# Optimization experiments

Hardware: AMD Instinct MI355X
Metric: run time of the kernel (lower is better)

Reference implementation:

```python
import jax, jax.numpy as jnp
import numpy as np

B, S, D, H, KV, HD = 2, 1024, 4096, 32, 8, 128
GROUP = H // KV


def setup_inputs() -> dict:
    key = jax.random.key(0)
    ks = jax.random.split(key, 9)
    x = jax.random.normal(ks[0], (B, S, D), dtype=jnp.float32)
    # RoPE tables: [max_seq_len, head_dim] (half-duplicated frequencies)
    pos = jnp.arange(S, dtype=jnp.float32)
    inv_freq = 1.0 / (10000.0 ** (jnp.arange(0, HD, 2, dtype=jnp.float32) / HD))
    freqs = pos[:, None] * inv_freq[None, :]            # [S, HD/2]
    emb = jnp.concatenate([freqs, freqs], axis=-1)      # [S, HD]
    cos, sin = jnp.cos(emb), jnp.sin(emb)
    # causal mask: True = masked
    mask = jnp.triu(jnp.ones((S, S), dtype=bool), 1)[None, None]  # [1,1,S,S]
    def qw(k, o, i):
        return jax.random.randint(k, (o, i), -127, 128, dtype=jnp.int8)
    wq = qw(ks[1], H * HD, D)
    wk = qw(ks[2], KV * HD, D)
    wv = qw(ks[3], KV * HD, D)
    wo = qw(ks[4], D, H * HD)
    sq = jnp.float32(0.02); sk = jnp.float32(0.02)
    sv = jnp.float32(0.02); so = jnp.float32(0.02)
    bq = jax.random.normal(ks[5], (H * HD,), jnp.float32) * 0.01
    bk = jax.random.normal(ks[6], (KV * HD,), jnp.float32) * 0.01
    bv = jax.random.normal(ks[7], (KV * HD,), jnp.float32) * 0.01
    return dict(x=x, mask=mask, cos=cos, sin=sin,
                wq=wq, bq=bq, sq=sq, wk=wk, bk=bk, sk=sk,
                wv=wv, bv=bv, sv=sv, wo=wo, so=so, start_pos=0)


def _deq_linear(x, w_int8, scale, bias):
    # dequantize-on-the-fly int8 linear: y = x @ (w.astype * scale).T + b
    w = w_int8.astype(x.dtype) * scale                  # [O, I]
    y = jnp.einsum('bsi,oi->bso', x, w)
    return y if bias is None else y + bias


def _rope(x, cos, sin, offset):
    # x: [b, s, h, hd]
    hd = x.shape[-1]
    x1, x2 = x[..., : hd // 2], x[..., hd // 2 :]
    s_len = x.shape[1]
    c = cos[offset : offset + s_len][None, :, None, :]
    s = sin[offset : offset + s_len][None, :, None, :]
    rotated = jnp.concatenate([-x2, x1], axis=-1)
    return (x * c + rotated * s).astype(x.dtype)


def reference(x, mask, cos, sin, wq, bq, sq, wk, bk, sk, wv, bv, sv, wo, so, start_pos):
    b, seq, _ = x.shape
    xq = _deq_linear(x, wq, sq, bq).reshape(b, seq, H, HD)
    xk = _deq_linear(x, wk, sk, bk).reshape(b, seq, KV, HD)
    xv = _deq_linear(x, wv, sv, bv).reshape(b, seq, KV, HD)
    xq = _rope(xq, cos, sin, start_pos)
    xk = _rope(xk, cos, sin, start_pos)
    # KV cache: start_pos=0 prefill -> cache[:start_pos+seq] == (xk, xv)
    kv_idx = jnp.arange(H) // GROUP                      # q head -> kv head
    keys = xk[:, :, kv_idx, :]                           # [b, kv_len, H, hd]
    values = xv[:, :, kv_idx, :]
    scores = jnp.einsum('bqhd,bkhd->bhqk', xq, keys) / np.sqrt(HD).astype(np.float32)
    scores = jnp.where(mask, -jnp.inf, scores)
    probs = jax.nn.softmax(scores, axis=-1)
    out = jnp.einsum('bhqk,bkhd->bqhd', probs, values).reshape(b, seq, H * HD)
    return _deq_linear(out, wo, so, None)
```

## Files before the change

kernel.cpp:

```cpp
#include <hip/hip_runtime.h>
#include <hip/hip_bf16.h>
#include <hip/hip_fp16.h>
#include <cstdint>

typedef _Float16 f16;
typedef _Float16 f16x8 __attribute__((ext_vector_type(8)));
typedef _Float16 f16x4 __attribute__((ext_vector_type(4)));
typedef float f32x4 __attribute__((ext_vector_type(4)));

#define DEV_INLINE __device__ __forceinline__

DEV_INLINE void async_ld16(const void* g, void* l) {
  __builtin_amdgcn_global_load_lds((const __attribute__((address_space(1))) void*)g,
                                   (__attribute__((address_space(3))) void*)l, 16, 0, 0);
}

template <int N>
DEV_INLINE void wait_vm() {
  static_assert(N >= 0 && N <= 12, "gate range");
  if constexpr (N == 0)  asm volatile("s_waitcnt vmcnt(0)" ::: "memory");
  if constexpr (N == 1)  asm volatile("s_waitcnt vmcnt(1)" ::: "memory");
  if constexpr (N == 2)  asm volatile("s_waitcnt vmcnt(2)" ::: "memory");
  if constexpr (N == 3)  asm volatile("s_waitcnt vmcnt(3)" ::: "memory");
  if constexpr (N == 4)  asm volatile("s_waitcnt vmcnt(4)" ::: "memory");
  if constexpr (N == 5)  asm volatile("s_waitcnt vmcnt(5)" ::: "memory");
  if constexpr (N == 6)  asm volatile("s_waitcnt vmcnt(6)" ::: "memory");
  if constexpr (N == 7)  asm volatile("s_waitcnt vmcnt(7)" ::: "memory");
  if constexpr (N == 8)  asm volatile("s_waitcnt vmcnt(8)" ::: "memory");
  if constexpr (N == 9)  asm volatile("s_waitcnt vmcnt(9)" ::: "memory");
  if constexpr (N == 10) asm volatile("s_waitcnt vmcnt(10)" ::: "memory");
  if constexpr (N == 11) asm volatile("s_waitcnt vmcnt(11)" ::: "memory");
  if constexpr (N == 12) asm volatile("s_waitcnt vmcnt(12)" ::: "memory");
}
DEV_INLINE void lgk0() {
  asm volatile("s_waitcnt lgkmcnt(0)" ::: "memory");
  __builtin_amdgcn_sched_barrier(0);
}

__global__ __launch_bounds__(256) void k_prep_all(
    const float* __restrict__ x,
    const int* __restrict__ wq, const int* __restrict__ wk, const int* __restrict__ wv,
    const float* __restrict__ bq, const float* __restrict__ bk, const float* __restrict__ bv,
    const float* __restrict__ sq, const float* __restrict__ sk, const float* __restrict__ sv,
    f16* __restrict__ acat, f16* __restrict__ wcat,
    float* __restrict__ bias_cat, float* __restrict__ scale_cat) {
  const int bid = blockIdx.x;
  if (bid < 8192) {
    int i = (bid * 256 + threadIdx.x) * 4;
    float4 v = *(const float4*)&x[i];
    int row = i >> 12, col = i & 4095;
    f16 h0 = (f16)v.x, h1 = (f16)v.y, h2 = (f16)v.z, h3 = (f16)v.w;
    f16x4 hi = {h0, h1, h2, h3};
    f16x4 lo = {(f16)(v.x - (float)h0), (f16)(v.y - (float)h1),
                (f16)(v.z - (float)h2), (f16)(v.w - (float)h3)};
    size_t base = (size_t)row * 8192 + col;
    *(f16x4*)&acat[base] = hi;
    *(f16x4*)&acat[base + 4096] = lo;
  } else {
    int i = (bid - 8192) * 256 + threadIdx.x;
    if (i < 6291456) {
      int e = i * 4, row = e >> 12, col = e & 4095;
      int4 v;
      if (row < 4096)      v = *(const int4*)&wq[(size_t)row * 4096 + col];
      else if (row < 5120) v = *(const int4*)&wk[(size_t)(row - 4096) * 4096 + col];
      else                 v = *(const int4*)&wv[(size_t)(row - 5120) * 4096 + col];
      f16x4 o = {(f16)(float)v.x, (f16)(float)v.y, (f16)(float)v.z, (f16)(float)v.w};
      *(f16x4*)&wcat[e] = o;
    }
    if (i < 6144) {
      float b, s;
      if (i < 4096)      { b = bq[i];        s = sq[0]; }
      else if (i < 5120) { b = bk[i - 4096]; s = sk[0]; }
      else               { b = bv[i - 5120]; s = sv[0]; }
      bias_cat[i] = b;
      scale_cat[i] = s;
    }
  }
}

__global__ __launch_bounds__(256) void k_cast_i32_f16(const int* __restrict__ w,
                                                      f16* __restrict__ out, int n) {
  int i = (blockIdx.x * 256 + threadIdx.x) * 4;
  if (i >= n) return;
  int4 v = *(const int4*)&w[i];
  f16x4 o = {(f16)(float)v.x, (f16)(float)v.y, (f16)(float)v.z, (f16)(float)v.w};
  *(f16x4*)&out[i] = o;
}

template <int BM, int BN, int MODE>
__global__ __launch_bounds__(512) void k_gemm9(
    const f16* __restrict__ A, const f16* __restrict__ W,
    f16* __restrict__ o_hi, f16* __restrict__ o_lo, float* __restrict__ o_f32,
    const float* __restrict__ scale_vec, const float* __restrict__ bias_vec,
    const float* __restrict__ scale_scalar,
    const float* __restrict__ cosT, const float* __restrict__ sinT,
    const int* __restrict__ sp,
    int N, int K, int kmask, int ldw, int nym) {
  constexpr int WM = 2, WN = 4;
  constexpr int MR = BM / WM / 16;
  constexpr int NR = BN / WN / 16;
  constexpr int AKC = BM * 64;
  constexpr int BKC = BN * 64;
  constexpr int SLOT = 2 * (AKC + BKC);
  constexpr int LAH = AKC / 8192;
  constexpr int LBH = BKC / 8192;
  constexpr int GS = 2 * (LAH + LBH);
  constexpr int G1 = LAH + LBH;
  extern __shared__ __align__(16) char lds[];

  const int t = threadIdx.x, w = t >> 6, ln = t & 63;
  const int lr = ln & 15, lg = ln >> 4;
  const int wn = w & 3, wm = w >> 2;

  const int nwg = gridDim.x;
  const int q8 = nwg >> 3, r8 = nwg & 7;
  const int xcd = blockIdx.x & 7, bidx = blockIdx.x >> 3;
  const int sid = (xcd < r8 ? xcd * (q8 + 1) : r8 * (q8 + 1) + (xcd - r8) * q8) + bidx;
  const int m0 = (sid % nym) * BM;
  const int n0 = (sid / nym) * BN;

  const f16* aSrc[LAH];
  const f16* bSrc[LBH];
#pragma unroll
  for (int l = 0; l < LAH; l++) {
    int ci = l * 512 + t, row = ci >> 2, c = ci & 3;
    aSrc[l] = A + (size_t)(m0 + row) * K + (c ^ ((row >> 1) & 3)) * 8;
  }
#pragma unroll
  for (int l = 0; l < LBH; l++) {
    int ci = l * 512 + t, row = ci >> 2, c = ci & 3;
    bSrc[l] = W + (size_t)(n0 + row) * ldw + (c ^ ((row >> 1) & 3)) * 8;
  }

  f32x4 acc[MR][NR] = {};
  f16x8 af[MR], bfa[NR];

  auto stageA = [&](int tt, int kc) {
    char* dst = lds + (tt & 1) * SLOT + kc * AKC;
    const int ko = tt * 64 + kc * 32;
#pragma unroll
    for (int l = 0; l < LAH; l++)
      async_ld16(aSrc[l] + ko, dst + (l * 512 + w * 64) * 16);
  };
  auto stageB = [&](int tt, int kc) {
    char* dst = lds + (tt & 1) * SLOT + 2 * AKC + kc * BKC;
    const int ko = ((tt * 64) & kmask) + kc * 32;
#pragma unroll
    for (int l = 0; l < LBH; l++)
      async_ld16(bSrc[l] + ko, dst + (l * 512 + w * 64) * 16);
  };
  auto readA = [&](int tt, int kc) {
    const char* base = lds + (tt & 1) * SLOT + kc * AKC;
#pragma unroll
    for (int mf = 0; mf < MR; mf++) {
      const int row = wm * (BM / WM) + mf * 16 + lr;
      af[mf] = *(const f16x8*)(base + row * 64 + (lg ^ ((row >> 1) & 3)) * 16);
    }
  };
  auto readBall = [&](int tt, int kc) {
    const char* base = lds + (tt & 1) * SLOT + 2 * AKC + kc * BKC;
#pragma unroll
    for (int nf = 0; nf < NR; nf++) {
      const int row = wn * (BN / WN) + nf * 16 + lr;
      bfa[nf] = *(const f16x8*)(base + row * 64 + (lg ^ ((row >> 1) & 3)) * 16);
    }
  };
  auto mma = [&]() {
    __builtin_amdgcn_s_setprio(1);
#pragma unroll
    for (int m = 0; m < MR; m++)
#pragma unroll
      for (int n = 0; n < NR; n++)
        acc[m][n] = __builtin_amdgcn_mfma_f32_16x16x32_f16(af[m], bfa[n], acc[m][n], 0, 0, 0);
    __builtin_amdgcn_s_setprio(0);
  };
  auto bar = [&]() { __builtin_amdgcn_s_barrier(); };

  const int NT = K >> 6;
  stageA(0, 0); stageB(0, 0); stageA(0, 1); stageB(0, 1);
  stageA(1, 0); stageB(1, 0);
  wait_vm<GS>();
  bar();

  for (int tt = 0; tt + 2 < NT; ++tt) {
    stageA(tt + 1, 1); stageB(tt + 1, 1);
    readA(tt, 0); readBall(tt, 0);
    wait_vm<GS>();
    bar(); lgk0(); mma(); bar();
    stageA(tt + 2, 0); stageB(tt + 2, 0);
    readA(tt, 1); readBall(tt, 1);
    wait_vm<GS>();
    bar(); lgk0(); mma(); bar();
  }
  {
    const int tt = NT - 2;
    stageA(tt + 1, 1); stageB(tt + 1, 1);
    readA(tt, 0); readBall(tt, 0);
    wait_vm<GS>();
    bar(); lgk0(); mma(); bar();
    readA(tt, 1); readBall(tt, 1);
    wait_vm<G1>();
    bar(); lgk0(); mma(); bar();
  }
  {
    const int tt = NT - 1;
    readA(tt, 0); readBall(tt, 0);
    wait_vm<0>();
    bar(); lgk0(); mma(); bar();
    readA(tt, 1); readBall(tt, 1);
    lgk0(); mma();
  }

  if constexpr (MODE == 0) {
    float* xch = (float*)lds;
    const int sp0 = sp[0];
    for (int pass = 0; pass < 2; ++pass) {
      bar();
      if (wm == pass) {
#pragma unroll
        for (int n = 0; n < NR; n++) {
          const int col = wn * (BN / WN) + n * 16 + lr;
          const float sc = scale_vec[n0 + col];
          const float bs = bias_vec[n0 + col];
#pragma unroll
          for (int m = 0; m < MR; m++)
#pragma unroll
            for (int r2 = 0; r2 < 4; r2++) {
              const int row = m * 16 + lg * 4 + r2;
              xch[row * 385 + col] = acc[m][n][r2] * sc + bs;
            }
        }
      }
      bar();
      for (int j = 0; j < (64 * BN) / 512; j++) {
        const int idx = j * 512 + t;
        const int r = idx / BN;
        const int c = idx - r * BN;
        const int gr = m0 + pass * 64 + r;
        const int gcol = n0 + c;
        float v = xch[r * 385 + c];
        float o;
        if (gcol < 5120) {
          const int q = c & 127;
          const int pos = (gr & 1023) + sp0;
          const float cs = cosT[pos * 128 + q];
          const float sn = sinT[pos * 128 + q];
          const float vp = xch[r * 385 + ((q < 64) ? c + 64 : c - 64)];
          o = (q < 64) ? v * cs - vp * sn : v * cs + vp * sn;
        } else {
          o = v;
        }
        f16 h = (f16)o;
        o_hi[(size_t)gr * N + gcol] = h;
        o_lo[(size_t)gr * N + gcol] = (f16)(o - (float)h);
      }
    }
  } else {
#pragma unroll
    for (int n = 0; n < NR; n++) {
      const int col = n0 + wn * (BN / WN) + n * 16 + lr;
      const float sc = scale_scalar[0];
#pragma unroll
      for (int m = 0; m < MR; m++)
#pragma unroll
        for (int r2 = 0; r2 < 4; r2++) {
          const int row = m0 + wm * (BM / WM) + m * 16 + lg * 4 + r2;
          o_f32[(size_t)row * N + col] = acc[m][n][r2] * sc;
        }
    }
  }
}

__global__ __launch_bounds__(512) void k_attn6(const f16* __restrict__ XH,
                                               const f16* __restrict__ XL,
                                               f16* __restrict__ out) {
  __shared__ __align__(16) f16 KsH[32 * 152];
  __shared__ __align__(16) f16 KsL[32 * 152];
  __shared__ __align__(16) f16 VT[128 * 40];
  __shared__ __align__(16) f16 Pb[8 * 16 * 40];
  const int t = threadIdx.x, w = t >> 6, l = t & 63;
  const int lr = l & 15, lg = l >> 4;
  const int id = blockIdx.x;
  const int kvh = id & 7;
  const int j = id >> 3;
  const int half = j >> 5;
  const int jj = j & 31;
  const int qb = half ? 7 - (jj >> 3) : (jj >> 3);
  const int hg = jj & 3;
  const int b = (jj >> 2) & 1;
  const int h = kvh * 4 + hg;
  const int q0 = qb * 128;
  const size_t rs_ = 6144;
  const f16* Qh = XH + ((size_t)(b * 1024 + q0)) * rs_ + h * 128;
  const f16* Ql_ = XL + ((size_t)(b * 1024 + q0)) * rs_ + h * 128;
  const f16* KhG = XH + ((size_t)(b * 1024)) * rs_ + 4096 + kvh * 128;
  const f16* KlG = XL + ((size_t)(b * 1024)) * rs_ + 4096 + kvh * 128;
  const f16* VG = XH + ((size_t)(b * 1024)) * rs_ + 5120 + kvh * 128;

  f16x8 qh[4], ql[4];
  {
    size_t qoff = (size_t)(w * 16 + lr) * rs_ + lg * 8;
#pragma unroll
    for (int c = 0; c < 4; c++) {
      qh[c] = *(const f16x8*)(Qh + qoff + c * 32);
      ql[c] = *(const f16x8*)(Ql_ + qoff + c * 32);
    }
  }
  f32x4 accd[8] = {};
  float m_r[4], l_r[4];
#pragma unroll
  for (int r = 0; r < 4; r++) { m_r[r] = -1e30f; l_r[r] = 0.f; }

  const int krow_s = t >> 4, kch = t & 15;
  const int vrow_s = t & 31, vd8 = t >> 5;
  f16x8 khr, klr, vr;
  auto loadKV = [&](int kv0) {
    size_t go = (size_t)(kv0 + krow_s) * rs_ + kch * 8;
    khr = *(const f16x8*)(KhG + go);
    klr = *(const f16x8*)(KlG + go);
    vr = *(const f16x8*)(VG + (size_t)(kv0 + vrow_s) * rs_ + vd8 * 8);
  };
  auto writeKV = [&]() {
    *(f16x8*)&KsH[krow_s * 152 + kch * 8] = khr;
    *(f16x8*)&KsL[krow_s * 152 + kch * 8] = klr;
#pragma unroll
    for (int jj2 = 0; jj2 < 8; jj2++) VT[(vd8 * 8 + jj2) * 40 + vrow_s] = vr[jj2];
  };

  const int nkv = q0 + 128;
  const int NT = nkv >> 5;
  loadKV(0);
  wait_vm<0>();
  writeKV();
  __syncthreads();

  for (int tt = 0; tt < NT; ++tt) {
    const int kv0 = tt * 32;
    const bool pf = (tt + 1 < NT);
    if (pf) {
      loadKV(kv0 + 32);
      __builtin_amdgcn_sched_barrier(0);
    }

    f32x4 sc[2] = {};
#pragma unroll
    for (int cb = 0; cb < 2; cb++)
#pragma unroll
      for (int c = 0; c < 4; c++) {
        const f16x8 kh = *(const f16x8*)&KsH[(cb * 16 + lr) * 152 + c * 32 + lg * 8];
        const f16x8 kl = *(const f16x8*)&KsL[(cb * 16 + lr) * 152 + c * 32 + lg * 8];
        sc[cb] = __builtin_amdgcn_mfma_f32_16x16x32_f16(qh[c], kh, sc[cb], 0, 0, 0);
        sc[cb] = __builtin_amdgcn_mfma_f32_16x16x32_f16(qh[c], kl, sc[cb], 0, 0, 0);
        sc[cb] = __builtin_amdgcn_mfma_f32_16x16x32_f16(ql[c], kh, sc[cb], 0, 0, 0);
      }

    const float scale = 0.088388347648318447f;
    float alpha[4], pv[2][4];
#pragma unroll
    for (int r = 0; r < 4; r++) {
      const int qg = q0 + w * 16 + lg * 4 + r;
      float mx = -1e30f;
#pragma unroll
      for (int cb = 0; cb < 2; cb++) {
        const int kg = kv0 + cb * 16 + lr;
        float s = sc[cb][r] * scale;
        s = (kg <= qg) ? s : -1e30f;
        pv[cb][r] = s;
        mx = fmaxf(mx, s);
      }
      mx = fmaxf(mx, __shfl_xor(mx, 1));
      mx = fmaxf(mx, __shfl_xor(mx, 2));
      mx = fmaxf(mx, __shfl_xor(mx, 4));
      mx = fmaxf(mx, __shfl_xor(mx, 8));
      const float mn = fmaxf(m_r[r], mx);
      alpha[r] = __expf(m_r[r] - mn);
      m_r[r] = mn;
      float rsum = 0.f;
#pragma unroll
      for (int cb = 0; cb < 2; cb++) {
        const int kg = kv0 + cb * 16 + lr;
        const float p = (kg <= qg) ? __expf(pv[cb][r] - mn) : 0.f;
        pv[cb][r] = p;
        rsum += p;
      }
      rsum += __shfl_xor(rsum, 1);
      rsum += __shfl_xor(rsum, 2);
      rsum += __shfl_xor(rsum, 4);
      rsum += __shfl_xor(rsum, 8);
      l_r[r] = l_r[r] * alpha[r] + rsum;
    }

    f16* Pw = &Pb[w * 16 * 40];
#pragma unroll
    for (int r = 0; r < 4; r++)
#pragma unroll
      for (int cb = 0; cb < 2; cb++)
        Pw[(lg * 4 + r) * 40 + cb * 16 + lr] = (f16)pv[cb][r];
    const f16x8 pf_ = *(const f16x8*)&Pw[lr * 40 + lg * 8];

#pragma unroll
    for (int dc = 0; dc < 8; dc++) {
      const f16x8 vf = *(const f16x8*)&VT[(dc * 16 + lr) * 40 + lg * 8];
#pragma unroll
      for (int r = 0; r < 4; r++) accd[dc][r] *= alpha[r];
      accd[dc] = __builtin_amdgcn_mfma_f32_16x16x32_f16(pf_, vf, accd[dc], 0, 0, 0);
    }

    __syncthreads();
    if (pf) writeKV();
    __syncthreads();
  }

#pragma unroll
  for (int dc = 0; dc < 8; dc++)
#pragma unroll
    for (int r = 0; r < 4; r++) {
      const int row = b * 1024 + q0 + w * 16 + lg * 4 + r;
      out[(size_t)row * 4096 + h * 128 + dc * 16 + lr] = (f16)(accd[dc][r] / l_r[r]);
    }
}

extern "C" void kernel_launch(void* const* d_in, const int* in_sizes, int n_in,
                              void* d_out, int out_size, void* d_ws, size_t ws_size,
                              hipStream_t stream) {
  const float* x = (const float*)d_in[0];
  const float* cosT = (const float*)d_in[2];
  const float* sinT = (const float*)d_in[3];
  const int* wq = (const int*)d_in[4];
  const float* bq = (const float*)d_in[5];
  const float* sq = (const float*)d_in[6];
  const int* wk = (const int*)d_in[7];
  const float* bk = (const float*)d_in[8];
  const float* sk = (const float*)d_in[9];
  const int* wv = (const int*)d_in[10];
  const float* bv = (const float*)d_in[11];
  const float* sv = (const float*)d_in[12];
  const int* wo = (const int*)d_in[13];
  const float* so = (const float*)d_in[14];
  const int* sp = (const int*)d_in[15];

  char* ws = (char*)d_ws;
  f16* Acat = (f16*)ws;
  f16* Wcat = (f16*)(ws + 33554432);
  f16* XH = (f16*)(ws + 83886080);
  f16* XL = (f16*)(ws + 109051904);
  f16* AO = (f16*)(ws + 134217728);
  float* biasv = (float*)(ws + 150994944);
  float* scalev = (float*)(ws + 151019520);

  hipFuncSetAttribute(reinterpret_cast<const void*>(&k_gemm9<128, 384, 0>),
                      hipFuncAttributeMaxDynamicSharedMemorySize, 131072);
  hipFuncSetAttribute(reinterpret_cast<const void*>(&k_gemm9<128, 256, 1>),
                      hipFuncAttributeMaxDynamicSharedMemorySize, 98304);

  k_prep_all<<<32768, 256, 0, stream>>>(x, wq, wk, wv, bq, bk, bv, sq, sk, sv,
                                        Acat, Wcat, biasv, scalev);

  k_gemm9<128, 384, 0><<<256, 512, 131072, stream>>>(
      Acat, Wcat, XH, XL, nullptr, scalev, biasv, nullptr, cosT, sinT, sp,
      6144, 8192, 4095, 4096, 16);

  f16* Wo_ = Acat;
  k_cast_i32_f16<<<16384, 256, 0, stream>>>(wo, Wo_, 16777216);

  k_attn6<<<512, 512, 0, stream>>>(XH, XL, AO);

  k_gemm9<128, 256, 1><<<256, 512, 98304, stream>>>(
      AO, Wo_, nullptr, nullptr, (float*)d_out, nullptr, nullptr, so,
      nullptr, nullptr, nullptr, 4096, 4096, 0x7fffffff, 4096, 16);
}
```

Before: 421.4 us.

## Replace QKV GEMM with dedicated 64x384-tile kernel and simpler double-buffered pipeline

Adds a dedicated QKV projection kernel that uses 64x384 tiles, 256 threads and 512 workgroups instead of 128x384 tiles with 512 threads. It uses a two-slot LDS pipeline with a K-step of 32 and an XCD-aware block-to-tile mapping, and keeps the fused bias, scale, RoPE and hi/lo f16 split epilogue. The generic GEMM is reduced to the output-projection mode only. The smaller tile and smaller LDS footprint are meant to improve occupancy and load balance across CUs, at the cost of less data reuse per tile and more redundant weight loads.

```diff
diff --git a/kernel.cpp b/kernel.cpp
--- a/kernel.cpp
+++ b/kernel.cpp
@@ -87,14 +87,154 @@
   *(f16x4*)&out[i] = o;
 }
 
+__global__ __launch_bounds__(256) void k_qkv10(
+    const f16* __restrict__ A, const f16* __restrict__ W,
+    f16* __restrict__ o_hi, f16* __restrict__ o_lo,
+    const float* __restrict__ scale_vec, const float* __restrict__ bias_vec,
+    const float* __restrict__ cosT, const float* __restrict__ sinT,
+    const int* __restrict__ sp) {
+  constexpr int BM = 64, BN = 384, N = 6144, K = 8192, kmask = 4095, ldw = 4096;
+  constexpr int MR = 4, NR = 6;
+  constexpr int AKC = BM * 64;
+  constexpr int BKC = BN * 64;
+  constexpr int SLOT = AKC + BKC;
+  constexpr int LB = 6;
+  extern __shared__ __align__(16) char lds[];
+
+  const int t = threadIdx.x, w = t >> 6, ln = t & 63;
+  const int lr = ln & 15, lg = ln >> 4;
+  const int wn = w;
+
+  const int xcd = blockIdx.x & 7, bidx = blockIdx.x >> 3;
+  const int sid = xcd * 64 + bidx;
+  const int m0 = (sid & 31) * BM;
+  const int n0 = (sid >> 5) * BN;
+
+  const f16* aSrc;
+  const f16* bSrc[LB];
+  {
+    int row = t >> 2, c = t & 3;
+    aSrc = A + (size_t)(m0 + row) * K + (c ^ ((row >> 1) & 3)) * 8;
+  }
+#pragma unroll
+  for (int l = 0; l < LB; l++) {
+    int ci = l * 256 + t, row = ci >> 2, c = ci & 3;
+    bSrc[l] = W + (size_t)(n0 + row) * ldw + (c ^ ((row >> 1) & 3)) * 8;
+  }
+
+  f32x4 acc[MR][NR] = {};
+  f16x8 af[MR], bfa[NR];
+
+  auto stage = [&](int tt) {
+    char* dst = lds + (tt & 1) * SLOT;
+    const int ko = tt * 32;
+    const int kb = ko & kmask;
+    async_ld16(aSrc + ko, dst + w * 1024);
+#pragma unroll
+    for (int l = 0; l < LB; l++)
+      async_ld16(bSrc[l] + kb, dst + AKC + (l * 256 + w * 64) * 16);
+  };
+  auto readAB = [&](int tt) {
+    const char* base = lds + (tt & 1) * SLOT;
+#pragma unroll
+    for (int mf = 0; mf < MR; mf++) {
+      const int row = mf * 16 + lr;
+      af[mf] = *(const f16x8*)(base + row * 64 + (lg ^ ((row >> 1) & 3)) * 16);
+    }
+    const char* bb = base + AKC;
+#pragma unroll
+    for (int nf = 0; nf < NR; nf++) {
+      const int row = wn * 96 + nf * 16 + lr;
+      bfa[nf] = *(const f16x8*)(bb + row * 64 + (lg ^ ((row >> 1) & 3)) * 16);
+    }
+  };
+  auto mma = [&]() {
+    __builtin_amdgcn_s_setprio(1);
+#pragma unroll
+    for (int m = 0; m < MR; m++)
+#pragma unroll
+      for (int n = 0; n < NR; n++)
+        acc[m][n] = __builtin_amdgcn_mfma_f32_16x16x32_f16(af[m], bfa[n], acc[m][n], 0, 0, 0);
+    __builtin_amdgcn_s_setprio(0);
+  };
+  auto bar = [&]() { __builtin_amdgcn_s_barrier(); };
+
+  constexpr int NT = K >> 5;
+  stage(0); stage(1);
+  wait_vm<7>();
+  bar();
+
+  for (int tt = 0; tt + 2 < NT; ++tt) {
+    readAB(tt);
+    lgk0();
+    bar();
+    stage(tt + 2);
+    mma();
+    wait_vm<7>();
+    bar();
+  }
+  {
+    readAB(NT - 2);
+    lgk0();
+    mma();
+    wait_vm<0>();
+    bar();
+  }
+  {
+    readAB(NT - 1);
+    lgk0();
+    mma();
+  }
+
+  float* xch = (float*)lds;
+  const int sp0 = sp[0];
+  for (int pass = 0; pass < 2; ++pass) {
+    bar();
+#pragma unroll
+    for (int mi = 0; mi < 2; ++mi) {
+      const int m = pass * 2 + mi;
+#pragma unroll
+      for (int n = 0; n < NR; n++) {
+        const int col = wn * 96 + n * 16 + lr;
+        const float sc = scale_vec[n0 + col];
+        const float bs = bias_vec[n0 + col];
+#pragma unroll
+        for (int r2 = 0; r2 < 4; r2++) {
+          const int xrow = mi * 16 + lg * 4 + r2;
+          xch[xrow * 385 + col] = acc[m][n][r2] * sc + bs;
+        }
+      }
+    }
+    bar();
+    for (int jj2 = 0; jj2 < 48; ++jj2) {
+      const int idx = jj2 * 256 + t;
+      const int r = idx / 384;
+      const int c = idx - r * 384;
+      const int gr = m0 + pass * 32 + r;
+      const int gcol = n0 + c;
+      float v = xch[r * 385 + c];
+      float o;
+      if (gcol < 5120) {
+        const int q = c & 127;
+        const int pos = (gr & 1023) + sp0;
+        const float cs = cosT[pos * 128 + q];
+        const float sn = sinT[pos * 128 + q];
+        const float vp = xch[r * 385 + ((q < 64) ? c + 64 : c - 64)];
+        o = (q < 64) ? v * cs - vp * sn : v * cs + vp * sn;
+      } else {
+        o = v;
+      }
+      f16 h = (f16)o;
+      o_hi[(size_t)gr * N + gcol] = h;
+      o_lo[(size_t)gr * N + gcol] = (f16)(o - (float)h);
+    }
+  }
+}
+
 template <int BM, int BN, int MODE>
 __global__ __launch_bounds__(512) void k_gemm9(
     const f16* __restrict__ A, const f16* __restrict__ W,
-    f16* __restrict__ o_hi, f16* __restrict__ o_lo, float* __restrict__ o_f32,
-    const float* __restrict__ scale_vec, const float* __restrict__ bias_vec,
-    const float* __restrict__ scale_scalar,
-    const float* __restrict__ cosT, const float* __restrict__ sinT,
-    const int* __restrict__ sp,
+    float* __restrict__ o_f32, const float* __restrict__ scale_scalar,
     int N, int K, int kmask, int ldw, int nym) {
   constexpr int WM = 2, WN = 4;
   constexpr int MR = BM / WM / 16;
@@ -211,63 +351,17 @@
     lgk0(); mma();
   }
 
-  if constexpr (MODE == 0) {
-    float* xch = (float*)lds;
-    const int sp0 = sp[0];
-    for (int pass = 0; pass < 2; ++pass) {
-      bar();
-      if (wm == pass) {
-#pragma unroll
-        for (int n = 0; n < NR; n++) {
-          const int col = wn * (BN / WN) + n * 16 + lr;
-          const float sc = scale_vec[n0 + col];
-          const float bs = bias_vec[n0 + col];
-#pragma unroll
-          for (int m = 0; m < MR; m++)
-#pragma unroll
-            for (int r2 = 0; r2 < 4; r2++) {
-              const int row = m * 16 + lg * 4 + r2;
-              xch[row * 385 + col] = acc[m][n][r2] * sc + bs;
-            }
-        }
+#pragma unroll
+  for (int n = 0; n < NR; n++) {
+    const int col = n0 + wn * (BN / WN) + n * 16 + lr;
+    const float sc = scale_scalar[0];
+#pragma unroll
+    for (int m = 0; m < MR; m++)
+#pragma unroll
+      for (int r2 = 0; r2 < 4; r2++) {
+        const int row = m0 + wm * (BM / WM) + m * 16 + lg * 4 + r2;
+        o_f32[(size_t)row * N + col] = acc[m][n][r2] * sc;
       }
-      bar();
-      for (int j = 0; j < (64 * BN) / 512; j++) {
-        const int idx = j * 512 + t;
-        const int r = idx / BN;
-        const int c = idx - r * BN;
-        const int gr = m0 + pass * 64 + r;
-        const int gcol = n0 + c;
-        float v = xch[r * 385 + c];
-        float o;
-        if (gcol < 5120) {
-          const int q = c & 127;
-          const int pos = (gr & 1023) + sp0;
-          const float cs = cosT[pos * 128 + q];
-          const float sn = sinT[pos * 128 + q];
-          const float vp = xch[r * 385 + ((q < 64) ? c + 64 : c - 64)];
-          o = (q < 64) ? v * cs - vp * sn : v * cs + vp * sn;
-        } else {
-          o = v;
-        }
-        f16 h = (f16)o;
-        o_hi[(size_t)gr * N + gcol] = h;
-        o_lo[(size_t)gr * N + gcol] = (f16)(o - (float)h);
-      }
-    }
-  } else {
-#pragma unroll
-    for (int n = 0; n < NR; n++) {
-      const int col = n0 + wn * (BN / WN) + n * 16 + lr;
-      const float sc = scale_scalar[0];
-#pragma unroll
-      for (int m = 0; m < MR; m++)
-#pragma unroll
-        for (int r2 = 0; r2 < 4; r2++) {
-          const int row = m0 + wm * (BM / WM) + m * 16 + lg * 4 + r2;
-          o_f32[(size_t)row * N + col] = acc[m][n][r2] * sc;
-        }
-    }
   }
 }
 
@@ -448,17 +542,16 @@
   float* biasv = (float*)(ws + 150994944);
   float* scalev = (float*)(ws + 151019520);
 
-  hipFuncSetAttribute(reinterpret_cast<const void*>(&k_gemm9<128, 384, 0>),
-                      hipFuncAttributeMaxDynamicSharedMemorySize, 131072);
+  hipFuncSetAttribute(reinterpret_cast<const void*>(&k_qkv10),
+                      hipFuncAttributeMaxDynamicSharedMemorySize, 57344);
   hipFuncSetAttribute(reinterpret_cast<const void*>(&k_gemm9<128, 256, 1>),
                       hipFuncAttributeMaxDynamicSharedMemorySize, 98304);
 
   k_prep_all<<<32768, 256, 0, stream>>>(x, wq, wk, wv, bq, bk, bv, sq, sk, sv,
                                         Acat, Wcat, biasv, scalev);
 
-  k_gemm9<128, 384, 0><<<256, 512, 131072, stream>>>(
-      Acat, Wcat, XH, XL, nullptr, scalev, biasv, nullptr, cosT, sinT, sp,
-      6144, 8192, 4095, 4096, 16);
+  k_qkv10<<<512, 256, 57344, stream>>>(Acat, Wcat, XH, XL, scalev, biasv,
+                                       cosT, sinT, sp);
 
   f16* Wo_ = Acat;
   k_cast_i32_f16<<<16384, 256, 0, stream>>>(wo, Wo_, 16777216);
@@ -466,6 +559,5 @@
   k_attn6<<<512, 512, 0, stream>>>(XH, XL, AO);
 
   k_gemm9<128, 256, 1><<<256, 512, 98304, stream>>>(
-      AO, Wo_, nullptr, nullptr, (float*)d_out, nullptr, nullptr, so,
-      nullptr, nullptr, nullptr, 4096, 4096, 0x7fffffff, 4096, 16);
-}
+      AO, Wo_, (float*)d_out, so, 4096, 4096, 0x7fffffff, 4096, 16);
+}
```

Result: slower. 483.0 us (+14.6%).
